# Optimization experiments

Hardware: AMD Instinct MI355X
Metric: run time of the kernel (lower is better)

Reference implementation:

```python
import jax, jax.numpy as jnp
import numpy as np
from functools import partial

D = 1024
H = 4 * D
E = 8
K_TOP = 2
B, T = 4, 2048
NEG_INF = jnp.float32(-1e30)


def setup_inputs() -> dict:
    key = jax.random.key(0)
    ks = jax.random.split(key, 12)
    s = 0.02
    return {
        "x": jax.random.normal(ks[0], (B, T, D), jnp.float32),
        "noise": jax.random.normal(ks[1], (B, T, E), jnp.float32),
        "gate_w": jax.random.normal(ks[2], (E, D), jnp.float32) * s,
        "gate_b": jnp.zeros((E,), jnp.float32),
        "var_w": jax.random.normal(ks[3], (E, D), jnp.float32) * s,
        "var_b": jnp.zeros((E,), jnp.float32),
        "w1": jax.random.normal(ks[4], (E, H, D), jnp.float32) * s,
        "b1": jnp.zeros((E, H), jnp.float32),
        "w2": jax.random.normal(ks[5], (E, D, H), jnp.float32) * s,
        "b2": jnp.zeros((E, D), jnp.float32),
    }


def reference(x, noise, gate_w, gate_b, var_w, var_b, w1, b1, w2, b2):
    # Noisy top-k gating
    logits = jnp.einsum("btd,ed->bte", x, gate_w) + gate_b          # [B,T,E]
    std = jax.nn.softplus(jnp.einsum("btd,ed->bte", x, var_w) + var_b)
    noisy = logits + noise * std                                      # [B,T,E]
    _, idx = jax.lax.top_k(noisy, K_TOP)                              # [B,T,K]
    # boolean top-k mask over experts
    mask = (idx[..., None] == jnp.arange(E)).any(axis=-2)             # [B,T,E]
    coef = jax.nn.softmax(jnp.where(mask, noisy, NEG_INF), axis=-1)   # zeros outside top-k

    # Combine: sum_e coef_e * FFN_e(x). coef is exactly 0 for non-selected
    # experts, so this equals the masked gather/scatter math. Scan over the
    # small expert dim to avoid a [E,B,T,H] intermediate.
    coef_e = jnp.moveaxis(coef, -1, 0)                                # [E,B,T]

    def body(acc, ew):
        w1e, b1e, w2e, b2e, ce = ew
        h = jax.nn.relu(jnp.einsum("btd,hd->bth", x, w1e) + b1e)
        y = jnp.einsum("bth,dh->btd", h, w2e) + b2e
        return acc + y * ce[..., None], None

    out, _ = jax.lax.scan(body, jnp.zeros_like(x), (w1, b1, w2, b2, coef_e))
    return out
```

## Files before the change

### kernel.cpp

```cpp
#include <hip/hip_runtime.h>
#include <hip/hip_bf16.h>
#include <math.h>

#define NTOK 8192
#define DD   1024
#define HH   4096
#define NE   8
#define BM 256
#define BN 256
#define SLOT_CAP (2 * NTOK + NE * BM)

typedef __bf16 bf16;
typedef __bf16 bf16x8 __attribute__((ext_vector_type(8)));
typedef __bf16 bf16x4 __attribute__((ext_vector_type(4)));
typedef float  f32x4  __attribute__((ext_vector_type(4)));

typedef __attribute__((address_space(3))) unsigned char lds_u8;
typedef const __attribute__((address_space(1))) unsigned char g_u8;

__device__ __forceinline__ void gload16(const bf16* g, bf16* l) {
  __builtin_amdgcn_global_load_lds((g_u8*)g, (lds_u8*)l, 16, 0, 0);
}

__device__ __forceinline__ float softplus_f(float v) {
  return fmaxf(v, 0.f) + log1pf(expf(-fabsf(v)));
}

__global__ __launch_bounds__(64) void moe_gate_kernel(
    const float* __restrict__ x, const float* __restrict__ noise,
    const float* __restrict__ gate_w, const float* __restrict__ gate_b,
    const float* __restrict__ var_w,  const float* __restrict__ var_b,
    float* __restrict__ coef2, int* __restrict__ t2e, int* __restrict__ counts)
{
  const int t = blockIdx.x;
  const int lane = threadIdx.x;
  const float* xt = x + (size_t)t * DD;
  float pg[NE], pv[NE];
  #pragma unroll
  for (int e = 0; e < NE; ++e) { pg[e] = 0.f; pv[e] = 0.f; }
  #pragma unroll 4
  for (int i = 0; i < DD / 64; ++i) {
    const int d = lane + i * 64;
    const float xv = xt[d];
    #pragma unroll
    for (int e = 0; e < NE; ++e) {
      pg[e] = fmaf(xv, gate_w[e * DD + d], pg[e]);
      pv[e] = fmaf(xv, var_w[e * DD + d], pv[e]);
    }
  }
  #pragma unroll
  for (int e = 0; e < NE; ++e) {
    #pragma unroll
    for (int off = 32; off; off >>= 1) {
      pg[e] += __shfl_xor(pg[e], off);
      pv[e] += __shfl_xor(pv[e], off);
    }
  }
  if (lane == 0) {
    float noisy[NE];
    #pragma unroll
    for (int e = 0; e < NE; ++e) {
      const float lg = pg[e] + gate_b[e];
      const float sd = softplus_f(pv[e] + var_b[e]);
      noisy[e] = lg + noise[t * NE + e] * sd;
    }
    int i1 = 0; float n1 = noisy[0];
    #pragma unroll
    for (int e = 1; e < NE; ++e) if (noisy[e] > n1) { n1 = noisy[e]; i1 = e; }
    int i2 = -1; float n2 = -3.0e38f;
    #pragma unroll
    for (int e = 0; e < NE; ++e) if (e != i1 && noisy[e] > n2) { n2 = noisy[e]; i2 = e; }
    const float e2 = expf(n2 - n1);
    const float den = 1.f + e2;
    coef2[t * 2 + 0] = 1.f / den;
    coef2[t * 2 + 1] = e2 / den;
    t2e[t * 2 + 0] = i1;
    t2e[t * 2 + 1] = i2;
    atomicAdd(&counts[i1], 1);
    atomicAdd(&counts[i2], 1);
  }
}

__global__ void moe_offsets_kernel(const int* __restrict__ counts, int* __restrict__ po) {
  if (threadIdx.x == 0) {
    int acc = 0;
    po[0] = 0;
    for (int e = 0; e < NE; ++e) {
      acc += ((counts[e] + BM - 1) / BM) * BM;
      po[e + 1] = acc;
    }
  }
}

__global__ __launch_bounds__(256) void moe_scatter_kernel(
    const int* __restrict__ t2e, const float* __restrict__ coef2,
    const int* __restrict__ po, int* __restrict__ cnt2,
    int* __restrict__ assign_tok, float* __restrict__ slot_coef)
{
  const int t = blockIdx.x * 256 + threadIdx.x;
  if (t >= NTOK) return;
  #pragma unroll
  for (int k = 0; k < 2; ++k) {
    const int e = t2e[t * 2 + k];
    const int pos = atomicAdd(&cnt2[e], 1);
    const int slot = po[e] + pos;
    assign_tok[slot] = t;
    slot_coef[slot] = coef2[t * 2 + k];
  }
}

__global__ __launch_bounds__(256) void cvt_bf16_kernel(const float* __restrict__ src,
                                                       bf16* __restrict__ dst, int n4) {
  for (int i = blockIdx.x * 256 + threadIdx.x; i < n4; i += gridDim.x * 256) {
    const float4 f = ((const float4*)src)[i];
    bf16x4 v;
    v[0] = (bf16)f.x; v[1] = (bf16)f.y; v[2] = (bf16)f.z; v[3] = (bf16)f.w;
    ((bf16x4*)dst)[i] = v;
  }
}

template<int KDIM, int KSTRIDE, int NCOLS, bool FFN1>
__global__ __launch_bounds__(512, 2) void moe_gemm8_kernel(
    const bf16* __restrict__ Asrc, const bf16* __restrict__ Wsrc,
    const float* __restrict__ bias,
    const int* __restrict__ assign_tok, const float* __restrict__ slot_coef,
    const int* __restrict__ po,
    bf16* __restrict__ hout, float* __restrict__ out,
    int chunk_base, int gx)
{
  constexpr int NI  = KDIM / 128;
  constexpr int KHT = KDIM / 32;
  __shared__ bf16 smA[32768];
  __shared__ bf16 smB[32768];
  __shared__ int toks[BM];

  const int nwg = gx * (NCOLS / BN);
  const int lin = blockIdx.x;
  const int q = nwg >> 3, r = nwg & 7;
  const int xcd = lin & 7, idx = lin >> 3;
  const int wg = (xcd < r ? xcd * (q + 1) : r * (q + 1) + (xcd - r) * q) + idx;
  const int bx = wg % gx, by = wg / gx;

  const int row0 = chunk_base + bx * BM;
  const int po8 = po[NE];
  if (row0 >= po8) return;
  int e = 0;
  while (row0 >= po[e + 1]) ++e;
  const int bn0 = by * BN;
  const size_t kbase = (size_t)blockIdx.z * KDIM;
  const bf16* We = Wsrc + (size_t)e * ((size_t)HH * DD) + kbase;
  const bf16* As = Asrc + kbase;

  const int tid = threadIdx.x, lane = tid & 63, wid = tid >> 6;
  if (tid < BM) toks[tid] = assign_tok[row0 + tid];
  __syncthreads();

  const int srcc = (((lane & 3) ^ ((lane >> 2) & 3)) * 8);
  const int rt0 = wid * 16 + (lane >> 2);
  const int rt1 = (8 + wid) * 16 + (lane >> 2);
  int ar0, ar1;
  if constexpr (FFN1) {
    const int s0 = toks[rt0]; ar0 = s0 < 0 ? 0 : s0;
    const int s1 = toks[rt1]; ar1 = s1 < 0 ? 0 : s1;
  } else {
    ar0 = row0 - chunk_base + rt0;
    ar1 = row0 - chunk_base + rt1;
  }
  const bf16* ap0 = As + (size_t)ar0 * KSTRIDE + srcc;
  const bf16* ap1 = As + (size_t)ar1 * KSTRIDE + srcc;
  const bf16* bp0 = We + (size_t)(bn0 + rt0) * KSTRIDE + srcc;
  const bf16* bp1 = We + (size_t)(bn0 + rt1) * KSTRIDE + srcc;

  auto stage = [&](int rr, int kh) {
    const int ko = kh * 32;
    gload16(ap0 + ko, &smA[rr * 8192 + wid * 512]);
    gload16(ap1 + ko, &smA[rr * 8192 + (8 + wid) * 512]);
    gload16(bp0 + ko, &smB[rr * 8192 + wid * 512]);
    gload16(bp1 + ko, &smB[rr * 8192 + (8 + wid) * 512]);
  };

  const int wr = wid >> 2, wc = wid & 3;
  const int la = lane & 15, hi = lane >> 4;
  const int cph = (hi ^ (la & 3)) * 8;
  const int aBase = wr * 4096 + la * 32 + cph;
  const int bBase = wc * 2048 + la * 32 + cph;

  f32x4 acc[8][4];
  #pragma unroll
  for (int m = 0; m < 8; ++m)
    #pragma unroll
    for (int n = 0; n < 4; ++n) acc[m][n] = {0.f, 0.f, 0.f, 0.f};

  stage(0, 0); stage(1, 1); stage(2, 2);

  for (int i = 0; i < NI; ++i) {
    #pragma unroll
    for (int pp = 0; pp < 4; ++pp) {
      asm volatile("s_waitcnt vmcnt(8)" ::: "memory");
      asm volatile("s_barrier" ::: "memory");
      bf16x8 a0[4], bb[4];
      #pragma unroll
      for (int m = 0; m < 4; ++m)
        a0[m] = *(const bf16x8*)(&smA[pp * 8192 + aBase + m * 512]);
      #pragma unroll
      for (int n = 0; n < 4; ++n)
        bb[n] = *(const bf16x8*)(&smB[pp * 8192 + bBase + n * 512]);
      stage((pp + 3) & 3, (i * 4 + 3 + pp) & (KHT - 1));
      __builtin_amdgcn_s_setprio(1);
      #pragma unroll
      for (int m = 0; m < 4; ++m)
        #pragma unroll
        for (int n = 0; n < 4; ++n)
          acc[m][n] = __builtin_amdgcn_mfma_f32_16x16x32_bf16(a0[m], bb[n], acc[m][n], 0, 0, 0);
      __builtin_amdgcn_s_setprio(0);
      bf16x8 a1[4];
      #pragma unroll
      for (int m = 0; m < 4; ++m)
        a1[m] = *(const bf16x8*)(&smA[pp * 8192 + aBase + (4 + m) * 512]);
      __builtin_amdgcn_s_setprio(1);
      #pragma unroll
      for (int m = 0; m < 4; ++m)
        #pragma unroll
        for (int n = 0; n < 4; ++n)
          acc[4 + m][n] = __builtin_amdgcn_mfma_f32_16x16x32_bf16(a1[m], bb[n], acc[4 + m][n], 0, 0, 0);
      __builtin_amdgcn_s_setprio(0);
    }
  }

  if constexpr (FFN1) {
    const int hrow0 = row0 - chunk_base;
    #pragma unroll
    for (int n = 0; n < 4; ++n) {
      const int col = bn0 + wc * 64 + n * 16 + la;
      const float bb = bias[e * NCOLS + col];
      #pragma unroll
      for (int m = 0; m < 8; ++m) {
        const int rl = wr * 128 + m * 16 + hi * 4;
        #pragma unroll
        for (int rr = 0; rr < 4; ++rr) {
          float v = acc[m][n][rr] + bb;
          v = v > 0.f ? v : 0.f;
          hout[(size_t)(hrow0 + rl + rr) * HH + col] = (bf16)v;
        }
      }
    }
  } else {
    const bool addb = (blockIdx.z == 0);
    #pragma unroll
    for (int n = 0; n < 4; ++n) {
      const int col = bn0 + wc * 64 + n * 16 + la;
      const float bb = addb ? bias[e * NCOLS + col] : 0.f;
      #pragma unroll
      for (int m = 0; m < 8; ++m) {
        const int rl = wr * 128 + m * 16 + hi * 4;
        #pragma unroll
        for (int rr = 0; rr < 4; ++rr) {
          const int tl = rl + rr;
          const int tok = toks[tl];
          if (tok >= 0) {
            const float c = slot_coef[row0 + tl];
            atomicAdd(out + (size_t)tok * DD + col, c * (acc[m][n][rr] + bb));
          }
        }
      }
    }
  }
}

extern "C" void kernel_launch(void* const* d_in, const int* in_sizes, int n_in,
                              void* d_out, int out_size, void* d_ws, size_t ws_size,
                              hipStream_t stream) {
  const float* x      = (const float*)d_in[0];
  const float* noise  = (const float*)d_in[1];
  const float* gate_w = (const float*)d_in[2];
  const float* gate_b = (const float*)d_in[3];
  const float* var_w  = (const float*)d_in[4];
  const float* var_b  = (const float*)d_in[5];
  const float* w1     = (const float*)d_in[6];
  const float* b1     = (const float*)d_in[7];
  const float* w2     = (const float*)d_in[8];
  const float* b2     = (const float*)d_in[9];
  float* out = (float*)d_out;
  (void)in_sizes; (void)n_in; (void)out_size;

  char* ws = (char*)d_ws;
  size_t off = 0;
  auto alloc = [&](size_t bytes) {
    off = (off + 255) & ~(size_t)255;
    size_t o = off;
    off += bytes;
    return o;
  };
  bf16*  xb         = (bf16*)(ws + alloc((size_t)NTOK * DD * 2));
  float* coef2      = (float*)(ws + alloc((size_t)NTOK * 2 * 4));
  int*   t2e        = (int*)(ws + alloc((size_t)NTOK * 2 * 4));
  int*   counts     = (int*)(ws + alloc(64));
  int*   cnt2       = counts + 8;
  int*   po         = (int*)(ws + alloc(64));
  int*   assign_tok = (int*)(ws + alloc((size_t)SLOT_CAP * 4));
  float* slot_coef  = (float*)(ws + alloc((size_t)SLOT_CAP * 4));
  bf16*  w1b        = (bf16*)(ws + alloc((size_t)NE * HH * DD * 2));
  bf16*  w2b        = (bf16*)(ws + alloc((size_t)NE * DD * HH * 2));
  off = (off + 255) & ~(size_t)255;
  const size_t h_avail = ws_size > off ? ws_size - off : 0;
  int chunk_rows = (int)(h_avail / ((size_t)HH * 2));
  chunk_rows = (chunk_rows / BM) * BM;
  if (chunk_rows < BM) chunk_rows = BM;
  if (chunk_rows > SLOT_CAP) chunk_rows = SLOT_CAP;
  bf16* hbuf = (bf16*)(ws + off);

  hipMemsetAsync(counts, 0, 64, stream);
  hipMemsetAsync(assign_tok, 0xFF, (size_t)SLOT_CAP * 4, stream);
  hipMemsetAsync(out, 0, (size_t)NTOK * DD * 4, stream);

  moe_gate_kernel<<<NTOK, 64, 0, stream>>>(x, noise, gate_w, gate_b, var_w, var_b,
                                           coef2, t2e, counts);
  moe_offsets_kernel<<<1, 64, 0, stream>>>(counts, po);
  moe_scatter_kernel<<<NTOK / 256, 256, 0, stream>>>(t2e, coef2, po, cnt2,
                                                     assign_tok, slot_coef);
  cvt_bf16_kernel<<<2048, 256, 0, stream>>>(x, xb, NTOK * DD / 4);
  cvt_bf16_kernel<<<2048, 256, 0, stream>>>(w1, w1b, NE * HH * DD / 4);
  cvt_bf16_kernel<<<2048, 256, 0, stream>>>(w2, w2b, NE * DD * HH / 4);

  const int rounds = (SLOT_CAP + chunk_rows - 1) / chunk_rows;
  for (int r = 0; r < rounds; ++r) {
    const int cb = r * chunk_rows;
    const int rows_here = (cb + chunk_rows <= SLOT_CAP) ? chunk_rows : (SLOT_CAP - cb);
    const int gx = rows_here / BM;
    dim3 g1(gx * (HH / BN), 1, 1);
    moe_gemm8_kernel<DD, DD, HH, true><<<g1, 512, 0, stream>>>(
        xb, w1b, b1, assign_tok, slot_coef, po, hbuf, nullptr, cb, gx);
    dim3 g2(gx * (DD / BN), 1, 2);
    moe_gemm8_kernel<HH / 2, HH, DD, false><<<g2, 512, 0, stream>>>(
        hbuf, w2b, b2, assign_tok, slot_coef, po, nullptr, out, cb, gx);
  }
}
```

Baseline: 952.5 us.

## Fuse x bf16 cast into gate, merge weight casts, restructure GEMM pipeline

The gate kernel now reads x as float4, writes the bf16 copy of x, and computes gate dot products with vectorized weight loads, which removes a separate conversion pass over x. The two weight conversions are merged into one launch. The GEMM main loop is rewritten with 64-wide K tiles split into halves, a new LDS swizzle, and loads interleaved between half-tile MFMA groups. FFN2 now uses a 4-way split-K instead of 2-way with a different block ordering. Together these aim to cut launch and memory-pass overhead and improve latency hiding, at the cost of more atomic/accumulation traffic on the output from the wider split-K.

```diff
diff --git a/kernel.cpp b/kernel.cpp
--- a/kernel.cpp
+++ b/kernel.cpp
@@ -30,22 +30,31 @@
     const float* __restrict__ x, const float* __restrict__ noise,
     const float* __restrict__ gate_w, const float* __restrict__ gate_b,
     const float* __restrict__ var_w,  const float* __restrict__ var_b,
-    float* __restrict__ coef2, int* __restrict__ t2e, int* __restrict__ counts)
+    float* __restrict__ coef2, int* __restrict__ t2e, int* __restrict__ counts,
+    bf16* __restrict__ xb)
 {
   const int t = blockIdx.x;
   const int lane = threadIdx.x;
-  const float* xt = x + (size_t)t * DD;
+  const float4* x4 = (const float4*)(x + (size_t)t * DD);
+  bf16x4* xb4 = (bf16x4*)(xb + (size_t)t * DD);
+  const float4* gw4 = (const float4*)gate_w;
+  const float4* vw4 = (const float4*)var_w;
   float pg[NE], pv[NE];
   #pragma unroll
   for (int e = 0; e < NE; ++e) { pg[e] = 0.f; pv[e] = 0.f; }
-  #pragma unroll 4
-  for (int i = 0; i < DD / 64; ++i) {
-    const int d = lane + i * 64;
-    const float xv = xt[d];
+  #pragma unroll
+  for (int i = 0; i < DD / 256; ++i) {
+    const int d4 = i * 64 + lane;
+    const float4 f = x4[d4];
+    bf16x4 v;
+    v[0] = (bf16)f.x; v[1] = (bf16)f.y; v[2] = (bf16)f.z; v[3] = (bf16)f.w;
+    xb4[d4] = v;
     #pragma unroll
     for (int e = 0; e < NE; ++e) {
-      pg[e] = fmaf(xv, gate_w[e * DD + d], pg[e]);
-      pv[e] = fmaf(xv, var_w[e * DD + d], pv[e]);
+      const float4 g = gw4[e * 256 + d4];
+      pg[e] = fmaf(f.x, g.x, fmaf(f.y, g.y, fmaf(f.z, g.z, fmaf(f.w, g.w, pg[e]))));
+      const float4 w = vw4[e * 256 + d4];
+      pv[e] = fmaf(f.x, w.x, fmaf(f.y, w.y, fmaf(f.z, w.z, fmaf(f.w, w.w, pv[e]))));
     }
   }
   #pragma unroll
@@ -109,15 +118,24 @@
   }
 }
 
-__global__ __launch_bounds__(256) void cvt_bf16_kernel(const float* __restrict__ src,
-                                                       bf16* __restrict__ dst, int n4) {
-  for (int i = blockIdx.x * 256 + threadIdx.x; i < n4; i += gridDim.x * 256) {
-    const float4 f = ((const float4*)src)[i];
+__global__ __launch_bounds__(256) void cvt2_bf16_kernel(
+    const float* __restrict__ s1, bf16* __restrict__ d1, int n41,
+    const float* __restrict__ s2, bf16* __restrict__ d2, int n42)
+{
+  for (int i = blockIdx.x * 256 + threadIdx.x; i < n41 + n42; i += gridDim.x * 256) {
+    const float* s = (i < n41) ? s1 : s2;
+    bf16* d = (i < n41) ? d1 : d2;
+    const int j = (i < n41) ? i : i - n41;
+    const float4 f = ((const float4*)s)[j];
     bf16x4 v;
     v[0] = (bf16)f.x; v[1] = (bf16)f.y; v[2] = (bf16)f.z; v[3] = (bf16)f.w;
-    ((bf16x4*)dst)[i] = v;
-  }
-}
+    ((bf16x4*)d)[j] = v;
+  }
+}
+
+#define VM8  asm volatile("s_waitcnt vmcnt(8)" ::: "memory")
+#define VM0  asm volatile("s_waitcnt vmcnt(0)" ::: "memory")
+#define BARR __builtin_amdgcn_s_barrier()
 
 template<int KDIM, int KSTRIDE, int NCOLS, bool FFN1>
 __global__ __launch_bounds__(512, 2) void moe_gemm8_kernel(
@@ -128,21 +146,23 @@
     bf16* __restrict__ hout, float* __restrict__ out,
     int chunk_base, int gx)
 {
-  constexpr int NI  = KDIM / 128;
-  constexpr int KHT = KDIM / 32;
+  constexpr int NT = KDIM / 64;
+  constexpr int NI = NT / 2;
   __shared__ bf16 smA[32768];
   __shared__ bf16 smB[32768];
   __shared__ int toks[BM];
 
-  const int nwg = gx * (NCOLS / BN);
+  const int nwg = gridDim.x;
   const int lin = blockIdx.x;
   const int q = nwg >> 3, r = nwg & 7;
   const int xcd = lin & 7, idx = lin >> 3;
   const int wg = (xcd < r ? xcd * (q + 1) : r * (q + 1) + (xcd - r) * q) + idx;
-  const int bx = wg % gx, by = wg / gx;
-
+  int bx, by;
+  if constexpr (FFN1) { bx = wg % gx; by = wg / gx; }
+  else               { by = wg % (NCOLS / BN); bx = wg / (NCOLS / BN); }
+
+  const int po8 = po[NE];
   const int row0 = chunk_base + bx * BM;
-  const int po8 = po[NE];
   if (row0 >= po8) return;
   int e = 0;
   while (row0 >= po[e + 1]) ++e;
@@ -155,35 +175,51 @@
   if (tid < BM) toks[tid] = assign_tok[row0 + tid];
   __syncthreads();
 
-  const int srcc = (((lane & 3) ^ ((lane >> 2) & 3)) * 8);
-  const int rt0 = wid * 16 + (lane >> 2);
-  const int rt1 = (8 + wid) * 16 + (lane >> 2);
+  const int r0 = tid >> 2, r1 = 128 + (tid >> 2);
+  const int cc = (((tid & 3) ^ ((tid >> 3) & 3)) * 8);
   int ar0, ar1;
   if constexpr (FFN1) {
-    const int s0 = toks[rt0]; ar0 = s0 < 0 ? 0 : s0;
-    const int s1 = toks[rt1]; ar1 = s1 < 0 ? 0 : s1;
+    const int s0 = toks[r0]; ar0 = s0 < 0 ? 0 : s0;
+    const int s1 = toks[r1]; ar1 = s1 < 0 ? 0 : s1;
   } else {
-    ar0 = row0 - chunk_base + rt0;
-    ar1 = row0 - chunk_base + rt1;
-  }
-  const bf16* ap0 = As + (size_t)ar0 * KSTRIDE + srcc;
-  const bf16* ap1 = As + (size_t)ar1 * KSTRIDE + srcc;
-  const bf16* bp0 = We + (size_t)(bn0 + rt0) * KSTRIDE + srcc;
-  const bf16* bp1 = We + (size_t)(bn0 + rt1) * KSTRIDE + srcc;
-
-  auto stage = [&](int rr, int kh) {
-    const int ko = kh * 32;
-    gload16(ap0 + ko, &smA[rr * 8192 + wid * 512]);
-    gload16(ap1 + ko, &smA[rr * 8192 + (8 + wid) * 512]);
-    gload16(bp0 + ko, &smB[rr * 8192 + wid * 512]);
-    gload16(bp1 + ko, &smB[rr * 8192 + (8 + wid) * 512]);
+    ar0 = row0 - chunk_base + r0;
+    ar1 = row0 - chunk_base + r1;
+  }
+  const bf16* pA0 = As + (size_t)ar0 * KSTRIDE + cc;
+  const bf16* pA1 = As + (size_t)ar1 * KSTRIDE + cc;
+  const bf16* pB0 = We + (size_t)(bn0 + r0) * KSTRIDE + cc;
+  const bf16* pB1 = We + (size_t)(bn0 + r1) * KSTRIDE + cc;
+
+  auto SA = [&](int buf, int h, int kt) {
+    const int ko = kt * 64 + h * 32;
+    bf16* d = smA + buf * 16384 + h * 8192 + tid * 8;
+    gload16(pA0 + ko, d);
+    gload16(pA1 + ko, d + 4096);
+  };
+  auto SB = [&](int buf, int h, int kt) {
+    const int ko = kt * 64 + h * 32;
+    bf16* d = smB + buf * 16384 + h * 8192 + tid * 8;
+    gload16(pB0 + ko, d);
+    gload16(pB1 + ko, d + 4096);
   };
 
   const int wr = wid >> 2, wc = wid & 3;
   const int la = lane & 15, hi = lane >> 4;
-  const int cph = (hi ^ (la & 3)) * 8;
-  const int aBase = wr * 4096 + la * 32 + cph;
-  const int bBase = wc * 2048 + la * 32 + cph;
+  const int cph = ((hi ^ ((la >> 1) & 3)) * 8);
+  const int aB = (wr * 128 + la) * 32 + cph;
+  const int bB = (wc * 64 + la) * 32 + cph;
+
+  bf16x8 aF[4], aG[4], bF[4];
+  auto RA = [&](bf16x8* d, int buf, int ks, int qq) {
+    #pragma unroll
+    for (int mm = 0; mm < 4; ++mm)
+      d[mm] = *(const bf16x8*)(smA + buf * 16384 + ks * 8192 + aB + qq * 2048 + mm * 512);
+  };
+  auto RB = [&](bf16x8* d, int buf, int ks) {
+    #pragma unroll
+    for (int n = 0; n < 4; ++n)
+      d[n] = *(const bf16x8*)(smB + buf * 16384 + ks * 8192 + bB + n * 512);
+  };
 
   f32x4 acc[8][4];
   #pragma unroll
@@ -191,41 +227,34 @@
     #pragma unroll
     for (int n = 0; n < 4; ++n) acc[m][n] = {0.f, 0.f, 0.f, 0.f};
 
-  stage(0, 0); stage(1, 1); stage(2, 2);
-
-  for (int i = 0; i < NI; ++i) {
-    #pragma unroll
-    for (int pp = 0; pp < 4; ++pp) {
-      asm volatile("s_waitcnt vmcnt(8)" ::: "memory");
-      asm volatile("s_barrier" ::: "memory");
-      bf16x8 a0[4], bb[4];
-      #pragma unroll
-      for (int m = 0; m < 4; ++m)
-        a0[m] = *(const bf16x8*)(&smA[pp * 8192 + aBase + m * 512]);
+  auto MM = [&](bf16x8* a, bf16x8* b, int mb) {
+    __builtin_amdgcn_s_setprio(1);
+    #pragma unroll
+    for (int mm = 0; mm < 4; ++mm)
       #pragma unroll
       for (int n = 0; n < 4; ++n)
-        bb[n] = *(const bf16x8*)(&smB[pp * 8192 + bBase + n * 512]);
-      stage((pp + 3) & 3, (i * 4 + 3 + pp) & (KHT - 1));
-      __builtin_amdgcn_s_setprio(1);
-      #pragma unroll
-      for (int m = 0; m < 4; ++m)
-        #pragma unroll
-        for (int n = 0; n < 4; ++n)
-          acc[m][n] = __builtin_amdgcn_mfma_f32_16x16x32_bf16(a0[m], bb[n], acc[m][n], 0, 0, 0);
-      __builtin_amdgcn_s_setprio(0);
-      bf16x8 a1[4];
-      #pragma unroll
-      for (int m = 0; m < 4; ++m)
-        a1[m] = *(const bf16x8*)(&smA[pp * 8192 + aBase + (4 + m) * 512]);
-      __builtin_amdgcn_s_setprio(1);
-      #pragma unroll
-      for (int m = 0; m < 4; ++m)
-        #pragma unroll
-        for (int n = 0; n < 4; ++n)
-          acc[4 + m][n] = __builtin_amdgcn_mfma_f32_16x16x32_bf16(a1[m], bb[n], acc[4 + m][n], 0, 0, 0);
-      __builtin_amdgcn_s_setprio(0);
-    }
-  }
+        acc[mb + mm][n] = __builtin_amdgcn_mfma_f32_16x16x32_bf16(a[mm], b[n], acc[mb + mm][n], 0, 0, 0);
+    __builtin_amdgcn_s_setprio(0);
+  };
+
+  SA(0, 0, 0); SB(0, 0, 0);
+  SA(0, 1, 0); SB(0, 1, 0);
+  SA(1, 0, 1); SB(1, 0, 1);
+
+  for (int t = 0; t < NI; ++t) {
+    const int t1 = 2 * t + 1;
+    const int w2 = (2 * t + 2) & (NT - 1);
+    const int w3 = (2 * t + 3) & (NT - 1);
+    VM8; BARR; RA(aF, 0, 0, 0); RB(bF, 0, 0); SA(1, 1, t1); MM(aF, bF, 0);
+    BARR; RA(aG, 0, 0, 1); SB(1, 1, t1); MM(aG, bF, 4);
+    VM8; BARR; RA(aF, 0, 1, 0); RB(bF, 0, 1); SA(0, 0, w2); MM(aF, bF, 0);
+    BARR; RA(aG, 0, 1, 1); SB(0, 0, w2); MM(aG, bF, 4);
+    VM8; BARR; RA(aF, 1, 0, 0); RB(bF, 1, 0); SA(0, 1, w2); MM(aF, bF, 0);
+    BARR; RA(aG, 1, 0, 1); SB(0, 1, w2); MM(aG, bF, 4);
+    VM8; BARR; RA(aF, 1, 1, 0); RB(bF, 1, 1); SA(1, 0, w3); MM(aF, bF, 0);
+    BARR; RA(aG, 1, 1, 1); SB(1, 0, w3); MM(aG, bF, 4);
+  }
+  VM0;
 
   if constexpr (FFN1) {
     const int hrow0 = row0 - chunk_base;
@@ -314,13 +343,12 @@
   hipMemsetAsync(out, 0, (size_t)NTOK * DD * 4, stream);
 
   moe_gate_kernel<<<NTOK, 64, 0, stream>>>(x, noise, gate_w, gate_b, var_w, var_b,
-                                           coef2, t2e, counts);
+                                           coef2, t2e, counts, xb);
   moe_offsets_kernel<<<1, 64, 0, stream>>>(counts, po);
   moe_scatter_kernel<<<NTOK / 256, 256, 0, stream>>>(t2e, coef2, po, cnt2,
                                                      assign_tok, slot_coef);
-  cvt_bf16_kernel<<<2048, 256, 0, stream>>>(x, xb, NTOK * DD / 4);
-  cvt_bf16_kernel<<<2048, 256, 0, stream>>>(w1, w1b, NE * HH * DD / 4);
-  cvt_bf16_kernel<<<2048, 256, 0, stream>>>(w2, w2b, NE * DD * HH / 4);
+  cvt2_bf16_kernel<<<2048, 256, 0, stream>>>(w1, w1b, NE * HH * DD / 4,
+                                             w2, w2b, NE * DD * HH / 4);
 
   const int rounds = (SLOT_CAP + chunk_rows - 1) / chunk_rows;
   for (int r = 0; r < rounds; ++r) {
@@ -330,8 +358,8 @@
     dim3 g1(gx * (HH / BN), 1, 1);
     moe_gemm8_kernel<DD, DD, HH, true><<<g1, 512, 0, stream>>>(
         xb, w1b, b1, assign_tok, slot_coef, po, hbuf, nullptr, cb, gx);
-    dim3 g2(gx * (DD / BN), 1, 2);
-    moe_gemm8_kernel<HH / 2, HH, DD, false><<<g2, 512, 0, stream>>>(
+    dim3 g2(gx * (DD / BN), 1, 4);
+    moe_gemm8_kernel<HH / 4, HH, DD, false><<<g2, 512, 0, stream>>>(
         hbuf, w2b, b2, assign_tok, slot_coef, po, nullptr, out, cb, gx);
   }
 }
```

After: 977.2 us. 2.6% more time.
